# Performance work log

Measured on AMD Instinct MI355X. Metric: run time of the kernel, lower is better.

Reference implementation:

```python
import jax, jax.numpy as jnp
import numpy as np

B, N, C = 2, 2048, 1024
H = 16
D = C // H  # head_dim = 64
SCALE = D ** -0.5


def setup_inputs() -> dict:
    key = jax.random.key(0)
    k1, k2, k3, k4 = jax.random.split(key, 4)
    x = jax.random.normal(k1, (B, N, C), dtype=jnp.float32)
    # nn.Linear(in_dim, 3*out_dim, bias=False): store as [in, 3*out] for x @ W
    w_qkv = jax.random.normal(k2, (C, 3 * C), dtype=jnp.float32) * (C ** -0.5)
    w_proj = jax.random.normal(k3, (C, C), dtype=jnp.float32) * (C ** -0.5)
    b_proj = jax.random.normal(k4, (C,), dtype=jnp.float32) * 0.01
    return {"x": x, "w_qkv": w_qkv, "w_proj": w_proj, "b_proj": b_proj}


def reference(x, w_qkv, w_proj, b_proj):
    b, n, c = x.shape
    # QKV projection -> [3, B, H, N, D]
    qkv = (x @ w_qkv).reshape(b, n, 3, H, D).transpose(2, 0, 3, 1, 4)
    q, k, v = qkv[0], qkv[1], qkv[2]
    # scaled dot-product attention, full [B, H, N, N] scores as in original
    attn = jax.nn.softmax(jnp.einsum('bhqd,bhkd->bhqk', q * SCALE, k), axis=-1)
    out = jnp.einsum('bhqk,bhkd->bhqd', attn, v)  # [B, H, N, D]
    out = out.transpose(0, 2, 1, 3).reshape(b, n, c)
    return out @ w_proj + b_proj
```

## Files before the change

### kernel.cpp

```cpp
#include <hip/hip_runtime.h>

typedef unsigned short u16;
typedef float f32x4 __attribute__((ext_vector_type(4)));
typedef short bf16x8 __attribute__((ext_vector_type(8)));
typedef u16 u16x4 __attribute__((ext_vector_type(4)));
typedef u16 u16x8 __attribute__((ext_vector_type(8)));
typedef __bf16 bfr4 __attribute__((ext_vector_type(4)));

#define BB 2
#define NN 2048
#define CC 1024
#define HH 16
#define DD 64
#define MM (BB * NN)
#define NQKV (3 * CC)
#define QSCALE 0.18033688011112042f

#if __has_builtin(__builtin_amdgcn_exp2f)
#define EXP2(x) __builtin_amdgcn_exp2f(x)
#else
#define EXP2(x) exp2f(x)
#endif

__device__ __forceinline__ u16 f2bf(float f) {
    unsigned u = __float_as_uint(f);
    u += 0x7FFFu + ((u >> 16) & 1u);
    return (u16)(u >> 16);
}

__device__ __forceinline__ void ld_lds16(const u16* g, u16* l) {
    __builtin_amdgcn_global_load_lds(
        (const __attribute__((address_space(1))) unsigned int*)g,
        (__attribute__((address_space(3))) unsigned int*)l, 16, 0, 0);
}

__global__ __launch_bounds__(256) void k_prep(const float* __restrict__ x,
                                              const float* __restrict__ wqkv,
                                              const float* __restrict__ wproj,
                                              u16* __restrict__ Xb,
                                              u16* __restrict__ Wq,
                                              u16* __restrict__ Wp) {
    __shared__ float tile[32][33];
    int bid = blockIdx.x, t = threadIdx.x;
    if (bid < 2048) {
        int i = (bid * 256 + t) * 8;
        float4 a = *(const float4*)(x + i);
        float4 b = *(const float4*)(x + i + 4);
        u16x8 o;
        o[0] = f2bf(a.x); o[1] = f2bf(a.y); o[2] = f2bf(a.z); o[3] = f2bf(a.w);
        o[4] = f2bf(b.x); o[5] = f2bf(b.y); o[6] = f2bf(b.z); o[7] = f2bf(b.w);
        *(u16x8*)(Xb + i) = o;
        return;
    }
    const float* in;
    u16* out;
    int Nn, n0, k0;
    if (bid < 2048 + 3072) {
        int b2 = bid - 2048;
        in = wqkv; out = Wq; Nn = NQKV;
        n0 = (b2 % 96) * 32; k0 = (b2 / 96) * 32;
    } else {
        int b3 = bid - 5120;
        in = wproj; out = Wp; Nn = CC;
        n0 = (b3 & 31) * 32; k0 = (b3 >> 5) * 32;
    }
    int tx = t & 31, ty = t >> 5;
#pragma unroll
    for (int r = 0; r < 32; r += 8)
        tile[ty + r][tx] = in[(size_t)(k0 + ty + r) * Nn + n0 + tx];
    __syncthreads();
#pragma unroll
    for (int r = 0; r < 32; r += 8)
        out[(size_t)(n0 + ty + r) * CC + k0 + tx] = f2bf(tile[tx][ty + r]);
}

__global__ __launch_bounds__(512, 2) void k_gemmq(
    const u16* __restrict__ A, const u16* __restrict__ B,
    u16* __restrict__ Qb, u16* __restrict__ Kb, u16* __restrict__ Vb) {
    const int Kd = 1024;
    __shared__ __align__(16) u16 Ah0[256][64], Bh0[192][64];
    __shared__ __align__(16) u16 Ah1[256][64], Bh1[192][64];

    int t = threadIdx.x, wave = t >> 6, lane = t & 63;
    int quad = lane >> 4, l16 = lane & 15;
    int wr = wave >> 2, wc = wave & 3;

    int cid = blockIdx.y * 16 + blockIdx.x;
    int swz = (cid & 7) * 32 + (cid >> 3);
    int m0 = (swz >> 4) * 256, n0 = (swz & 15) * 192;

    int strow = wave * 8 + (lane >> 3);
    int stdst = (lane & 7) * 8;
    int stsrc = ((lane & 7) ^ (lane >> 3)) * 8;

    f32x4 acc[8][3];
#pragma unroll
    for (int i = 0; i < 8; i++)
#pragma unroll
        for (int j = 0; j < 3; j++) acc[i][j] = f32x4{0.f, 0.f, 0.f, 0.f};

    auto STAGE = [&](int k0, u16 (*Ad)[64], u16 (*Bd)[64]) {
#pragma unroll
        for (int i = 0; i < 4; i++) {
            int row = i * 64 + strow;
            ld_lds16(A + (size_t)(m0 + row) * Kd + k0 + stsrc, &Ad[row][stdst]);
        }
#pragma unroll
        for (int i = 0; i < 3; i++) {
            int row = i * 64 + strow;
            ld_lds16(B + (size_t)(n0 + row) * Kd + k0 + stsrc, &Bd[row][stdst]);
        }
    };
    auto COMPUTE = [&](u16 (*As)[64], u16 (*Bs)[64]) {
#pragma unroll
        for (int s = 0; s < 2; s++) {
            int pos = ((s * 4 + quad) ^ (l16 & 7)) * 8;
            bf16x8 af[8], bg[3];
#pragma unroll
            for (int m = 0; m < 8; m++)
                af[m] = *(const bf16x8*)&As[wr * 128 + m * 16 + l16][pos];
#pragma unroll
            for (int n = 0; n < 3; n++)
                bg[n] = *(const bf16x8*)&Bs[wc * 48 + n * 16 + l16][pos];
            __builtin_amdgcn_s_setprio(1);
#pragma unroll
            for (int m = 0; m < 8; m++)
#pragma unroll
                for (int n = 0; n < 3; n++)
                    acc[m][n] = __builtin_amdgcn_mfma_f32_16x16x32_bf16(
                        af[m], bg[n], acc[m][n], 0, 0, 0);
            __builtin_amdgcn_s_setprio(0);
        }
    };

    STAGE(0, Ah0, Bh0);
    __syncthreads();
    for (int k0 = 0; k0 < Kd; k0 += 128) {
        STAGE(k0 + 64, Ah1, Bh1);
        COMPUTE(Ah0, Bh0);
        __syncthreads();
        if (k0 + 128 < Kd) STAGE(k0 + 128, Ah0, Bh0);
        COMPUTE(Ah1, Bh1);
        __syncthreads();
    }

#pragma unroll
    for (int m = 0; m < 8; m++)
#pragma unroll
        for (int n = 0; n < 3; n++)
#pragma unroll
            for (int r = 0; r < 4; r++) {
                int grow = m0 + wr * 128 + m * 16 + quad * 4 + r;
                int gcol = n0 + wc * 48 + n * 16 + l16;
                float v = acc[m][n][r];
                int three = gcol >> 10, rem = gcol & 1023;
                int h = rem >> 6, d = rem & 63;
                int bb = grow >> 11, nn = grow & 2047;
                if (three == 0) {
                    Qb[((size_t)(bb * HH + h) * NN + nn) * DD + d] = f2bf(v * QSCALE);
                } else if (three == 1) {
                    Kb[((size_t)(bb * HH + h) * NN + nn) * DD + d] = f2bf(v);
                } else {
                    Vb[((size_t)(bb * HH + h) * DD + d) * NN + nn] = f2bf(v);
                }
            }
}

__global__ __launch_bounds__(256) void k_gemmp(
    const u16* __restrict__ A, const u16* __restrict__ B,
    const float* __restrict__ bias, float* __restrict__ Cout) {
    const int Kd = 1024;
    __shared__ __align__(16) u16 Ah0[64][64], Bh0[128][64];
    __shared__ __align__(16) u16 Ah1[64][64], Bh1[128][64];

    int t = threadIdx.x, wave = t >> 6, lane = t & 63;
    int quad = lane >> 4, l16 = lane & 15;
    int m0 = blockIdx.x * 64, n0 = blockIdx.y * 128;

    int strow = wave * 8 + (lane >> 3);
    int stdst = (lane & 7) * 8;
    int stsrc = ((lane & 7) ^ (lane >> 3)) * 8;

    f32x4 acc[4][2];
#pragma unroll
    for (int i = 0; i < 4; i++)
#pragma unroll
        for (int j = 0; j < 2; j++) acc[i][j] = f32x4{0.f, 0.f, 0.f, 0.f};

    auto STAGE = [&](int k0, u16 (*Ad)[64], u16 (*Bd)[64]) {
#pragma unroll
        for (int i = 0; i < 2; i++) {
            int row = i * 32 + strow;
            ld_lds16(A + (size_t)(m0 + row) * Kd + k0 + stsrc, &Ad[row][stdst]);
        }
#pragma unroll
        for (int i = 0; i < 4; i++) {
            int row = i * 32 + strow;
            ld_lds16(B + (size_t)(n0 + row) * Kd + k0 + stsrc, &Bd[row][stdst]);
        }
    };
    auto COMPUTE = [&](u16 (*As)[64], u16 (*Bs)[64]) {
#pragma unroll
        for (int s = 0; s < 2; s++) {
            int pos = ((s * 4 + quad) ^ (l16 & 7)) * 8;
            bf16x8 af[4], bg[2];
#pragma unroll
            for (int m = 0; m < 4; m++)
                af[m] = *(const bf16x8*)&As[m * 16 + l16][pos];
#pragma unroll
            for (int n = 0; n < 2; n++)
                bg[n] = *(const bf16x8*)&Bs[wave * 32 + n * 16 + l16][pos];
            __builtin_amdgcn_s_setprio(1);
#pragma unroll
            for (int m = 0; m < 4; m++)
#pragma unroll
                for (int n = 0; n < 2; n++)
                    acc[m][n] = __builtin_amdgcn_mfma_f32_16x16x32_bf16(
                        af[m], bg[n], acc[m][n], 0, 0, 0);
            __builtin_amdgcn_s_setprio(0);
        }
    };

    STAGE(0, Ah0, Bh0);
    __syncthreads();
    for (int k0 = 0; k0 < Kd; k0 += 128) {
        STAGE(k0 + 64, Ah1, Bh1);
        COMPUTE(Ah0, Bh0);
        __syncthreads();
        if (k0 + 128 < Kd) STAGE(k0 + 128, Ah0, Bh0);
        COMPUTE(Ah1, Bh1);
        __syncthreads();
    }

#pragma unroll
    for (int m = 0; m < 4; m++)
#pragma unroll
        for (int n = 0; n < 2; n++)
#pragma unroll
            for (int r = 0; r < 4; r++) {
                int grow = m0 + m * 16 + quad * 4 + r;
                int gcol = n0 + wave * 32 + n * 16 + l16;
                Cout[(size_t)grow * CC + gcol] = acc[m][n][r] + bias[gcol];
            }
}

__global__ __launch_bounds__(512) void k_attn(const u16* __restrict__ Qb,
                                              const u16* __restrict__ Kb,
                                              const u16* __restrict__ VbT,
                                              u16* __restrict__ Ob) {
    __shared__ __align__(16) u16 Ks0[64][64], Ks1[64][64];
    __shared__ __align__(16) u16 Vs0[64][64], Vs1[64][64];
    __shared__ __align__(16) u16 Ps[8][16][72];

    int t = threadIdx.x, wave = t >> 6, lane = t & 63;
    int quad = lane >> 4, l16 = lane & 15;
    int bh = blockIdx.x, q0 = blockIdx.y * 128;
    const size_t kbase = (size_t)bh * NN * DD;
    const size_t vbase = (size_t)bh * DD * NN;

    int qrow = q0 + wave * 16 + l16;
    bf16x8 qf0 = *(const bf16x8*)&Qb[kbase + (size_t)qrow * DD + quad * 8];
    bf16x8 qf1 = *(const bf16x8*)&Qb[kbase + (size_t)qrow * DD + 32 + quad * 8];

    f32x4 o[4];
#pragma unroll
    for (int i = 0; i < 4; i++) o[i] = f32x4{0.f, 0.f, 0.f, 0.f};
    f32x4 lrow = f32x4{0.f, 0.f, 0.f, 0.f};

    int stgrp = lane & 7;
    int stsrc = (stgrp ^ (lane >> 3)) * 8;
    int strow = wave * 8 + (lane >> 3);
    int cf0 = (quad ^ (l16 & 7)) * 8;
    int cf1 = ((4 + quad) ^ (l16 & 7)) * 8;

    auto STAGE = [&](int cc, u16 (*Kd_)[64], u16 (*Vd_)[64]) {
        ld_lds16(&Kb[kbase + (size_t)(cc * 64 + strow) * DD + stsrc],
                 &Kd_[strow][stgrp * 8]);
        ld_lds16(&VbT[vbase + (size_t)strow * NN + cc * 64 + stsrc],
                 &Vd_[strow][stgrp * 8]);
    };

    auto COMPUTE = [&](u16 (*Ksrc)[64], u16 (*Vsrc)[64]) {
        bf16x8 kf[4][2];
#pragma unroll
        for (int kt = 0; kt < 4; kt++) {
            kf[kt][0] = *(const bf16x8*)&Ksrc[kt * 16 + l16][cf0];
            kf[kt][1] = *(const bf16x8*)&Ksrc[kt * 16 + l16][cf1];
        }
        f32x4 s[4];
        __builtin_amdgcn_s_setprio(1);
#pragma unroll
        for (int kt = 0; kt < 4; kt++) {
            f32x4 z = f32x4{0.f, 0.f, 0.f, 0.f};
            z = __builtin_amdgcn_mfma_f32_16x16x32_bf16(kf[kt][0], qf0, z, 0, 0, 0);
            z = __builtin_amdgcn_mfma_f32_16x16x32_bf16(kf[kt][1], qf1, z, 0, 0, 0);
            s[kt] = z;
        }
        __builtin_amdgcn_s_setprio(0);
#pragma unroll
        for (int kt = 0; kt < 4; kt++) {
            bfr4 pk;
#pragma unroll
            for (int r = 0; r < 4; r++) {
                float e = EXP2(s[kt][r]);
                lrow[r] += e;
                pk[r] = (__bf16)e;
            }
            *(bfr4*)&Ps[wave][l16][kt * 16 + quad * 4] = pk;
        }
        __asm__ volatile("s_waitcnt lgkmcnt(0)" ::: "memory");
        bf16x8 pb0 = *(const bf16x8*)&Ps[wave][l16][quad * 8];
        bf16x8 pb1 = *(const bf16x8*)&Ps[wave][l16][32 + quad * 8];
        __builtin_amdgcn_s_setprio(1);
#pragma unroll
        for (int dt = 0; dt < 4; dt++) {
            bf16x8 vf0 = *(const bf16x8*)&Vsrc[dt * 16 + l16][cf0];
            bf16x8 vf1 = *(const bf16x8*)&Vsrc[dt * 16 + l16][cf1];
            o[dt] = __builtin_amdgcn_mfma_f32_16x16x32_bf16(vf0, pb0, o[dt], 0, 0, 0);
            o[dt] = __builtin_amdgcn_mfma_f32_16x16x32_bf16(vf1, pb1, o[dt], 0, 0, 0);
        }
        __builtin_amdgcn_s_setprio(0);
    };

    STAGE(0, Ks0, Vs0);
    __syncthreads();

    for (int c = 0; c < NN / 64; c += 2) {
        STAGE(c + 1, Ks1, Vs1);
        COMPUTE(Ks0, Vs0);
        __syncthreads();
        if (c + 2 < NN / 64) STAGE(c + 2, Ks0, Vs0);
        COMPUTE(Ks1, Vs1);
        __syncthreads();
    }

    int b = bh >> 4, h = bh & 15;
    float l = (lrow[0] + lrow[1]) + (lrow[2] + lrow[3]);
    l += __shfl_xor(l, 16, 64);
    l += __shfl_xor(l, 32, 64);
    float inv = 1.f / l;
    int grow = b * NN + q0 + wave * 16 + l16;
#pragma unroll
    for (int dt = 0; dt < 4; dt++) {
        u16x4 hv;
#pragma unroll
        for (int r = 0; r < 4; r++) hv[r] = f2bf(o[dt][r] * inv);
        int gcol = h * DD + dt * 16 + quad * 4;
        *(u16x4*)&Ob[(size_t)grow * CC + gcol] = hv;
    }
}

extern "C" void kernel_launch(void* const* d_in, const int* in_sizes, int n_in,
                              void* d_out, int out_size, void* d_ws, size_t ws_size,
                              hipStream_t stream) {
    const float* x      = (const float*)d_in[0];
    const float* w_qkv  = (const float*)d_in[1];
    const float* w_proj = (const float*)d_in[2];
    const float* b_proj = (const float*)d_in[3];
    float* out = (float*)d_out;

    u16* p = (u16*)d_ws;
    u16* Xb = p; p += (size_t)MM * CC;
    u16* Wq = p; p += (size_t)NQKV * CC;
    u16* Wp = p; p += (size_t)CC * CC;
    u16* Qb = p; p += (size_t)MM * CC;
    u16* Kb = p; p += (size_t)MM * CC;
    u16* Vb = p; p += (size_t)MM * CC;
    u16* Ob = p; p += (size_t)MM * CC;

    k_prep<<<2048 + 3072 + 1024, 256, 0, stream>>>(x, w_qkv, w_proj, Xb, Wq, Wp);
    k_gemmq<<<dim3(NQKV / 192, MM / 256), 512, 0, stream>>>(Xb, Wq, Qb, Kb, Vb);
    k_attn<<<dim3(BB * HH, NN / 128), 512, 0, stream>>>(Qb, Kb, Vb, Ob);
    k_gemmp<<<dim3(MM / 64, CC / 128), 256, 0, stream>>>(Ob, Wp, b_proj, out);
}
```

Baseline: 186.3 us.

## Replace double-buffered 64-K staging in output projection GEMM with single-buffered 128-K tile

The projection GEMM drops its two 64-wide K double buffers and uses one 128-wide K tile per iteration, with a sync before and after each stage. This halves the number of loop iterations and changes the LDS swizzle to fit 16 chunks per row. In exchange, global-to-LDS loads no longer overlap with MFMA compute, since each stage has to finish before compute starts.

```diff
diff --git a/kernel.cpp b/kernel.cpp
--- a/kernel.cpp
+++ b/kernel.cpp
@@ -170,16 +170,15 @@
     const u16* __restrict__ A, const u16* __restrict__ B,
     const float* __restrict__ bias, float* __restrict__ Cout) {
     const int Kd = 1024;
-    __shared__ __align__(16) u16 Ah0[64][64], Bh0[128][64];
-    __shared__ __align__(16) u16 Ah1[64][64], Bh1[128][64];
+    __shared__ __align__(16) u16 Ah[64][128];
+    __shared__ __align__(16) u16 Bh[128][128];
 
     int t = threadIdx.x, wave = t >> 6, lane = t & 63;
     int quad = lane >> 4, l16 = lane & 15;
     int m0 = blockIdx.x * 64, n0 = blockIdx.y * 128;
 
-    int strow = wave * 8 + (lane >> 3);
-    int stdst = (lane & 7) * 8;
-    int stsrc = ((lane & 7) ^ (lane >> 3)) * 8;
+    int strow = lane >> 4;
+    int stdst = (lane & 15) * 8;
 
     f32x4 acc[4][2];
 #pragma unroll
@@ -187,29 +186,31 @@
 #pragma unroll
         for (int j = 0; j < 2; j++) acc[i][j] = f32x4{0.f, 0.f, 0.f, 0.f};
 
-    auto STAGE = [&](int k0, u16 (*Ad)[64], u16 (*Bd)[64]) {
-#pragma unroll
-        for (int i = 0; i < 2; i++) {
-            int row = i * 32 + strow;
-            ld_lds16(A + (size_t)(m0 + row) * Kd + k0 + stsrc, &Ad[row][stdst]);
-        }
+    auto STAGE = [&](int k0) {
 #pragma unroll
         for (int i = 0; i < 4; i++) {
-            int row = i * 32 + strow;
-            ld_lds16(B + (size_t)(n0 + row) * Kd + k0 + stsrc, &Bd[row][stdst]);
-        }
-    };
-    auto COMPUTE = [&](u16 (*As)[64], u16 (*Bs)[64]) {
-#pragma unroll
-        for (int s = 0; s < 2; s++) {
+            int row = wave * 16 + i * 4 + strow;
+            int src = ((lane & 15) ^ (row & 7)) * 8;
+            ld_lds16(A + (size_t)(m0 + row) * Kd + k0 + src, &Ah[row & 63][0] + stdst);
+        }
+#pragma unroll
+        for (int i = 0; i < 8; i++) {
+            int row = wave * 32 + i * 4 + strow;
+            int src = ((lane & 15) ^ (row & 7)) * 8;
+            ld_lds16(B + (size_t)(n0 + row) * Kd + k0 + src, &Bh[row & 127][0] + stdst);
+        }
+    };
+    auto COMPUTE = [&]() {
+#pragma unroll
+        for (int s = 0; s < 4; s++) {
             int pos = ((s * 4 + quad) ^ (l16 & 7)) * 8;
             bf16x8 af[4], bg[2];
 #pragma unroll
             for (int m = 0; m < 4; m++)
-                af[m] = *(const bf16x8*)&As[m * 16 + l16][pos];
+                af[m] = *(const bf16x8*)&Ah[m * 16 + l16][pos];
 #pragma unroll
             for (int n = 0; n < 2; n++)
-                bg[n] = *(const bf16x8*)&Bs[wave * 32 + n * 16 + l16][pos];
+                bg[n] = *(const bf16x8*)&Bh[wave * 32 + n * 16 + l16][pos];
             __builtin_amdgcn_s_setprio(1);
 #pragma unroll
             for (int m = 0; m < 4; m++)
@@ -221,15 +222,11 @@
         }
     };
 
-    STAGE(0, Ah0, Bh0);
-    __syncthreads();
     for (int k0 = 0; k0 < Kd; k0 += 128) {
-        STAGE(k0 + 64, Ah1, Bh1);
-        COMPUTE(Ah0, Bh0);
-        __syncthreads();
-        if (k0 + 128 < Kd) STAGE(k0 + 128, Ah0, Bh0);
-        COMPUTE(Ah1, Bh1);
-        __syncthreads();
+        __syncthreads();
+        STAGE(k0);
+        __syncthreads();
+        COMPUTE();
     }
 
 #pragma unroll
```

New measurement: 184.3 us. About the same (-1.1%).
